# Optimization experiments

Measured on AMD Instinct MI355X. Metric: run time of the kernel, lower is better.

## Reference

```python
import jax, jax.numpy as jnp
import numpy as np

V, E, H2 = 32000, 512, 1024  # vocab, embed dim, lstm hidden (hidden_dim*2)
H = 512                      # attention inner dim (hidden_dim)
B, S = 64, 128
L = 2


def _lstm_cell(x, h, c, w_ih, w_hh, b_ih, b_hh):
    # PyTorch gate order: i, f, g, o
    gates = x @ w_ih.T + b_ih + h @ w_hh.T + b_hh
    i, f, g, o = jnp.split(gates, 4, axis=-1)
    i = jax.nn.sigmoid(i); f = jax.nn.sigmoid(f)
    g = jnp.tanh(g); o = jax.nn.sigmoid(o)
    c_new = f * c + i * g
    h_new = o * jnp.tanh(c_new)
    return h_new, c_new


def setup_inputs() -> dict:
    key = jax.random.key(0)
    ks = jax.random.split(key, 20)
    s = 0.05
    inp = {
        'input_token': jax.random.randint(ks[0], (B,), 0, V, dtype=jnp.int32),
        'hidden': jax.random.normal(ks[1], (L, B, H2), jnp.float32),
        'cell': jax.random.normal(ks[2], (L, B, H2), jnp.float32),
        'encoder_outputs': jax.random.normal(ks[3], (B, S, H2), jnp.float32),
        'mask': jax.random.randint(ks[4], (B, S), 0, 2, dtype=jnp.int32),
        'emb_table': jax.random.normal(ks[5], (V, E), jnp.float32) * s,
        'attn_w': jax.random.normal(ks[6], (H, 4 * H), jnp.float32) * s,
        'attn_b': jnp.zeros((H,), jnp.float32),
        'v_w': jax.random.normal(ks[7], (1, H), jnp.float32) * s,
        'w_ih0': jax.random.normal(ks[8], (4 * H2, E + H2), jnp.float32) * s,
        'w_hh0': jax.random.normal(ks[9], (4 * H2, H2), jnp.float32) * s,
        'b_ih0': jnp.zeros((4 * H2,), jnp.float32),
        'b_hh0': jnp.zeros((4 * H2,), jnp.float32),
        'w_ih1': jax.random.normal(ks[10], (4 * H2, H2), jnp.float32) * s,
        'w_hh1': jax.random.normal(ks[11], (4 * H2, H2), jnp.float32) * s,
        'b_ih1': jnp.zeros((4 * H2,), jnp.float32),
        'b_hh1': jnp.zeros((4 * H2,), jnp.float32),
        'fc_w': jax.random.normal(ks[12], (V, 4 * H + E), jnp.float32) * s,
        'fc_b': jnp.zeros((V,), jnp.float32),
    }
    return inp


def reference(input_token, hidden, cell, encoder_outputs, mask,
              emb_table, attn_w, attn_b, v_w,
              w_ih0, w_hh0, b_ih0, b_hh0,
              w_ih1, w_hh1, b_ih1, b_hh1,
              fc_w, fc_b):
    embedded = emb_table[input_token]                       # [B, E]
    h_top = hidden[-1]                                      # [B, 2H]
    # Bahdanau additive attention
    h_rep = jnp.broadcast_to(h_top[:, None, :], (B, S, H2))
    energy = jnp.tanh(jnp.concatenate([h_rep, encoder_outputs], axis=2) @ attn_w.T + attn_b)  # [B,S,H]
    attention = energy @ v_w[0]                             # [B, S]
    attention = jnp.where(mask == 0, jnp.float32(-1e10), attention)
    attn_weights = jax.nn.softmax(attention, axis=1)
    context = jnp.einsum('bs,bsd->bd', attn_weights, encoder_outputs)  # [B, 2H]
    # single-step 2-layer LSTM
    x = jnp.concatenate([embedded, context], axis=1)        # [B, E+2H]
    h0, c0 = _lstm_cell(x, hidden[0], cell[0], w_ih0, w_hh0, b_ih0, b_hh0)
    h1, c1 = _lstm_cell(h0, hidden[1], cell[1], w_ih1, w_hh1, b_ih1, b_hh1)
    new_hidden = jnp.stack([h0, h1])
    new_cell = jnp.stack([c0, c1])
    prediction = jnp.concatenate([h1, context, embedded], axis=1) @ fc_w.T + fc_b  # [B, V]
    return prediction, new_hidden, new_cell, attn_weights
```

## Files before the change

kernel.cpp:

```cpp
#include <hip/hip_runtime.h>


typedef __attribute__((ext_vector_type(8))) short bf16x8;
typedef __attribute__((ext_vector_type(4))) float f32x4;

__device__ __forceinline__ short f2bf(float f){
  __bf16 h = (__bf16)f;
  return __builtin_bit_cast(short, h);
}

__device__ __forceinline__ bf16x8 cvt8(float4 a, float4 b){
  bf16x8 r;
  r[0]=f2bf(a.x); r[1]=f2bf(a.y); r[2]=f2bf(a.z); r[3]=f2bf(a.w);
  r[4]=f2bf(b.x); r[5]=f2bf(b.y); r[6]=f2bf(b.z); r[7]=f2bf(b.w);
  return r;
}

__device__ __forceinline__ bf16x8 ld8_bf(const float* __restrict__ p){
  return cvt8(*(const float4*)p, *(const float4*)(p + 4));
}

__device__ __forceinline__ float fast_tanh(float x){
  x = fminf(fmaxf(x, -15.f), 15.f);
  float t = __expf(2.f * x);
  return (t - 1.f) / (t + 1.f);
}
__device__ __forceinline__ float fast_sig(float x){
  return 1.f / (1.f + __expf(-x));
}

__device__ __forceinline__ void stage16(const void* src, void* dst_lds){
  __builtin_amdgcn_global_load_lds(
      (const __attribute__((address_space(1))) void*)src,
      (__attribute__((address_space(3))) void*)dst_lds, 16, 0, 0);
}

__device__ __forceinline__ void gates_body(
    const short* __restrict__ A, int lda,
    const float* __restrict__ W1, int sW1, int K1,
    const float* __restrict__ W2, int sW2,
    float* __restrict__ Pplane, int N, int nb, int k0, char* smem)
{
  short* Al = (short*)smem;
  float* Wl = (float*)(smem + 32768);
  const int wv   = threadIdx.x >> 6;
  const int lane = threadIdx.x & 63;
  const int l15  = lane & 15;
  const int lg   = lane >> 4;

  const float* W; int sW, koff;
  if (k0 < K1){ W = W1; sW = sW1; koff = k0; }
  else        { W = W2; sW = sW2; koff = k0 - K1; }

  {
    const int r2  = lane >> 5;
    const int c16 = (lane & 31) * 16;
    #pragma unroll
    for (int i = 0; i < 8; ++i){
      int rbase = wv*16 + i*2;
      int row   = rbase + r2;
      const char* src = (const char*)A + (long)row*lda*2 + (long)k0*2
                        + (c16 ^ ((row & 7) << 4));
      stage16(src, (void*)(Al + rbase*256));
    }
  }

  auto STAGEW = [&](int bi, int kbase){
    #pragma unroll
    for (int i = 0; i < 4; ++i){
      int row = wv*16 + i*4 + lg;
      const char* src = (const char*)(W + (long)(nb + row)*sW + koff + kbase)
                        + ((l15*16) ^ ((row & 7) << 4));
      stage16(src, (void*)(Wl + bi*4096 + (wv*16 + i*4)*64));
    }
  };

  STAGEW(0, 0);
  STAGEW(1, 64);
  asm volatile("s_waitcnt vmcnt(8)" ::: "memory");
  asm volatile("s_barrier" ::: "memory");

  f32x4 acc[4];
  #pragma unroll
  for (int m = 0; m < 4; ++m) acc[m] = (f32x4){0.f,0.f,0.f,0.f};

  const int  rl = wv*16 + l15;
  const int  sw = (l15 & 7) << 4;
  const char* wbase = (const char*)Wl;
  const char* abase = (const char*)Al;

  auto COMPUTE = [&](int bi, int t){
    bf16x8 a[4][2];
    #pragma unroll
    for (int m = 0; m < 4; ++m)
      #pragma unroll
      for (int h = 0; h < 2; ++h){
        int cb = t*128 + h*64 + lg*16;
        a[m][h] = *(const bf16x8*)(abase + (m*16 + l15)*512 + (cb ^ sw));
      }
    const char* rb = wbase + bi*16384 + rl*256;
    float4 w00 = *(const float4*)(rb + ((lg*32      ) ^ sw));
    float4 w01 = *(const float4*)(rb + ((lg*32 + 16 ) ^ sw));
    float4 w10 = *(const float4*)(rb + ((lg*32 + 128) ^ sw));
    float4 w11 = *(const float4*)(rb + ((lg*32 + 144) ^ sw));
    bf16x8 wf0 = cvt8(w00, w01);
    bf16x8 wf1 = cvt8(w10, w11);
    #pragma unroll
    for (int m = 0; m < 4; ++m)
      acc[m] = __builtin_amdgcn_mfma_f32_16x16x32_bf16(a[m][0], wf0, acc[m], 0,0,0);
    #pragma unroll
    for (int m = 0; m < 4; ++m)
      acc[m] = __builtin_amdgcn_mfma_f32_16x16x32_bf16(a[m][1], wf1, acc[m], 0,0,0);
  };

  asm volatile("s_waitcnt vmcnt(4)" ::: "memory");
  COMPUTE(0, 0);
  STAGEW(2, 128);
  asm volatile("s_waitcnt vmcnt(4)" ::: "memory");
  COMPUTE(1, 1);
  STAGEW(0, 192);
  asm volatile("s_waitcnt vmcnt(4)" ::: "memory");
  COMPUTE(2, 2);
  asm volatile("s_waitcnt vmcnt(0)" ::: "memory");
  COMPUTE(0, 3);

  #pragma unroll
  for (int mt = 0; mt < 4; ++mt)
    #pragma unroll
    for (int r = 0; r < 4; ++r){
      int m = mt*16 + lg*4 + r;
      Pplane[(long)m * N + nb + wv*16 + l15] = acc[mt][r];
    }
}

__device__ __forceinline__ void fc_body(
    const short* __restrict__ A, int lda,
    const float* __restrict__ W, int sW, int NC,
    const float* __restrict__ addsrc, const float* __restrict__ bias,
    float* __restrict__ C, int N, int nb, char* smem)
{
  short* Al = (short*)smem;
  float* Wl = (float*)(smem + 32768);
  const int wv   = threadIdx.x >> 6;
  const int lane = threadIdx.x & 63;
  const int l15  = lane & 15;
  const int lg   = lane >> 4;

  auto STAGEA = [&](int c){
    short* dst = Al + (c & 1) * 8192;
    #pragma unroll
    for (int i = 0; i < 4; ++i){
      int rbase = wv*16 + i*4;
      int row   = rbase + lg;
      const char* src = (const char*)(A + (long)row*lda + c*128)
                        + ((l15*16) ^ ((row & 7) << 4));
      stage16(src, (void*)(dst + rbase*128));
    }
  };
  auto STAGEW = [&](int s){
    float* dst = Wl + (s % 3) * 4096;
    #pragma unroll
    for (int i = 0; i < 4; ++i){
      int row = wv*16 + i*4 + lg;
      const char* src = (const char*)(W + (long)(nb + row)*sW + s*64)
                        + ((l15*16) ^ ((row & 7) << 4));
      stage16(src, (void*)(dst + (wv*16 + i*4)*64));
    }
  };

  f32x4 acc[4];
  #pragma unroll
  for (int m = 0; m < 4; ++m) acc[m] = (f32x4){0.f,0.f,0.f,0.f};

  const int rl = wv*16 + l15;
  const int sw = (l15 & 7) << 4;

  auto COMPUTE = [&](int s){
    const char* abase = (const char*)(Al + ((s >> 1) & 1) * 8192);
    const int   kh    = (s & 1) * 128;
    bf16x8 a[4][2];
    #pragma unroll
    for (int m = 0; m < 4; ++m)
      #pragma unroll
      for (int h = 0; h < 2; ++h){
        int cb = kh + h*64 + lg*16;
        a[m][h] = *(const bf16x8*)(abase + (m*16 + l15)*256 + (cb ^ sw));
      }
    const char* rb = (const char*)(Wl + (s % 3)*4096) + rl*256;
    float4 w00 = *(const float4*)(rb + ((lg*32      ) ^ sw));
    float4 w01 = *(const float4*)(rb + ((lg*32 + 16 ) ^ sw));
    float4 w10 = *(const float4*)(rb + ((lg*32 + 128) ^ sw));
    float4 w11 = *(const float4*)(rb + ((lg*32 + 144) ^ sw));
    bf16x8 wf0 = cvt8(w00, w01);
    bf16x8 wf1 = cvt8(w10, w11);
    #pragma unroll
    for (int m = 0; m < 4; ++m)
      acc[m] = __builtin_amdgcn_mfma_f32_16x16x32_bf16(a[m][0], wf0, acc[m], 0,0,0);
    #pragma unroll
    for (int m = 0; m < 4; ++m)
      acc[m] = __builtin_amdgcn_mfma_f32_16x16x32_bf16(a[m][1], wf1, acc[m], 0,0,0);
  };

  STAGEA(0); STAGEW(0); STAGEW(1);
  asm volatile("s_waitcnt vmcnt(4)" ::: "memory");
  __builtin_amdgcn_s_barrier();

  STAGEA(1);
  COMPUTE(0);
  STAGEW(2);
  asm volatile("s_waitcnt vmcnt(4)" ::: "memory");
  COMPUTE(1);
  STAGEW(3);
  __builtin_amdgcn_s_barrier();

  for (int c = 1; c < NC-1; ++c){
    STAGEA(c+1);
    asm volatile("s_waitcnt vmcnt(8)" ::: "memory");
    COMPUTE(2*c);
    STAGEW(2*c+2);
    asm volatile("s_waitcnt vmcnt(4)" ::: "memory");
    COMPUTE(2*c+1);
    STAGEW(2*c+3);
    __builtin_amdgcn_s_barrier();
  }

  asm volatile("s_waitcnt vmcnt(4)" ::: "memory");
  COMPUTE(2*NC-2);
  asm volatile("s_waitcnt vmcnt(0)" ::: "memory");
  COMPUTE(2*NC-1);

  const int col = nb + wv*16 + l15;
  const float bn = bias ? bias[col] : 0.f;
  #pragma unroll
  for (int mt = 0; mt < 4; ++mt)
    #pragma unroll
    for (int r = 0; r < 4; ++r){
      int m = mt*16 + lg*4 + r;
      long idx = (long)m * N + col;
      float v = acc[mt][r] + bn;
      if (addsrc) v += addsrc[idx];
      C[idx] = v;
    }
}

__global__ __launch_bounds__(256) void prep_all(
    const int* __restrict__ tok, const float* __restrict__ emb,
    const float* __restrict__ hidden, const float* __restrict__ enc,
    const float* __restrict__ attn_w, const float* __restrict__ attn_b,
    short* __restrict__ encbf, short* __restrict__ Wbf,
    short* __restrict__ A0, short* __restrict__ A1, short* __restrict__ Zb,
    float* __restrict__ sco, float* __restrict__ hpr)
{
  const int bid = blockIdx.x, t = threadIdx.x;
  if (bid < 8){
    const int wv = t >> 6, lane = t & 63, l15 = lane & 15, lg = lane >> 4;
    const int nb = bid*64 + wv*16;
    const float* hrow = hidden + 65536;
    const float* wrow = attn_w + (long)(nb + l15)*2048 + lg*8;
    f32x4 acc[4] = {};
    bf16x8 wn  = ld8_bf(wrow);
    bf16x8 an0 = ld8_bf(hrow + l15*1024 + lg*8);
    bf16x8 an1 = ld8_bf(hrow + (16+l15)*1024 + lg*8);
    bf16x8 an2 = ld8_bf(hrow + (32+l15)*1024 + lg*8);
    bf16x8 an3 = ld8_bf(hrow + (48+l15)*1024 + lg*8);
    for (int kb = 32; kb < 1024; kb += 32){
      bf16x8 wc = wn, c0 = an0, c1 = an1, c2 = an2, c3 = an3;
      wn  = ld8_bf(wrow + kb);
      an0 = ld8_bf(hrow + l15*1024 + lg*8 + kb);
      an1 = ld8_bf(hrow + (16+l15)*1024 + lg*8 + kb);
      an2 = ld8_bf(hrow + (32+l15)*1024 + lg*8 + kb);
      an3 = ld8_bf(hrow + (48+l15)*1024 + lg*8 + kb);
      acc[0] = __builtin_amdgcn_mfma_f32_16x16x32_bf16(c0, wc, acc[0], 0,0,0);
      acc[1] = __builtin_amdgcn_mfma_f32_16x16x32_bf16(c1, wc, acc[1], 0,0,0);
      acc[2] = __builtin_amdgcn_mfma_f32_16x16x32_bf16(c2, wc, acc[2], 0,0,0);
      acc[3] = __builtin_amdgcn_mfma_f32_16x16x32_bf16(c3, wc, acc[3], 0,0,0);
    }
    acc[0] = __builtin_amdgcn_mfma_f32_16x16x32_bf16(an0, wn, acc[0], 0,0,0);
    acc[1] = __builtin_amdgcn_mfma_f32_16x16x32_bf16(an1, wn, acc[1], 0,0,0);
    acc[2] = __builtin_amdgcn_mfma_f32_16x16x32_bf16(an2, wn, acc[2], 0,0,0);
    acc[3] = __builtin_amdgcn_mfma_f32_16x16x32_bf16(an3, wn, acc[3], 0,0,0);
    const float bn = attn_b[nb + l15];
    #pragma unroll
    for (int mt = 0; mt < 4; ++mt)
      #pragma unroll
      for (int r = 0; r < 4; ++r)
        hpr[(mt*16 + lg*4 + r)*512 + nb + l15] = acc[mt][r] + bn;
  } else if (bid < 4104){
    long i = ((long)(bid-8)*256 + t)*8;
    *(bf16x8*)(encbf + i) = ld8_bf(enc + i);
  } else if (bid < 4360){
    int j = (bid-4104)*256 + t;
    int r = j >> 7, c = (j & 127)*8;
    *(bf16x8*)(Wbf + r*1024 + c) = ld8_bf(attn_w + (long)r*2048 + 1024 + c);
  } else if (bid < 4376){
    int j = (bid-4360)*256 + t;
    int b = j >> 6, e8 = (j & 63)*8;
    bf16x8 v = ld8_bf(emb + (long)tok[b]*512 + e8);
    *(bf16x8*)(A0 + b*2560 + e8) = v;
    *(bf16x8*)(Zb + b*2560 + 2048 + e8) = v;
  } else if (bid < 4408){
    int j = (bid-4376)*256 + t;
    int b = j >> 7, n8 = (j & 127)*8;
    *(bf16x8*)(A0 + b*2560 + 1536 + n8) = ld8_bf(hidden + (long)b*1024 + n8);
    *(bf16x8*)(A1 + b*2048 + 1024 + n8) = ld8_bf(hidden + 65536 + (long)b*1024 + n8);
  } else {
    int j = (bid-4408)*256 + t;
    float4 z = {0.f, 0.f, 0.f, 0.f};
    *(float4*)(sco + j*8) = z;
    *(float4*)(sco + j*8 + 4) = z;
  }
}

__global__ __launch_bounds__(256) void energy_lds(
    const short* __restrict__ encbf, const short* __restrict__ Wbf,
    const float* __restrict__ hpr, const float* __restrict__ v_w,
    float* __restrict__ scores)
{
  __shared__ short Ab[3][64*64];
  __shared__ short Bb[3][64*64];
  const int bx   = blockIdx.x;
  const int m3   = bx & 127, n3 = bx >> 7;
  const int wv   = threadIdx.x >> 6;
  const int lane = threadIdx.x & 63;
  const int l15  = lane & 15;
  const int lg   = lane >> 4;
  const int mb   = m3 * 64;
  const int nbg  = n3 * 64;
  const int nb   = nbg + wv * 16;
  const int b    = mb >> 7;

  const float hp = hpr[(long)b*512 + nb + l15];
  const float vn = v_w[nb + l15];

  const int srow = lane >> 3;
  const int scb  = (lane & 7) * 16;

  auto STAGE = [&](int c, int kb){
    short* da = Ab[c % 3];
    short* db = Bb[c % 3];
    #pragma unroll
    for (int i = 0; i < 2; ++i){
      int rbase = wv*16 + i*8;
      int row   = rbase + srow;
      int swz   = scb ^ ((row & 7) << 4);
      const char* sa = (const char*)(encbf + (long)(mb + row)*1024 + kb) + swz;
      stage16(sa, (void*)(da + rbase*64));
      const char* sb = (const char*)(Wbf + (long)(nbg + row)*1024 + kb) + swz;
      stage16(sb, (void*)(db + rbase*64));
    }
  };

  f32x4 acc[4] = {};
  const int brow = wv*16 + l15;
  const int bswz = (brow & 7) << 4;
  const int aswz = (l15 & 7) << 4;

  auto COMPUTE = [&](int c){
    const char* ab = (const char*)Ab[c % 3];
    const char* bb = (const char*)Bb[c % 3];
    #pragma unroll
    for (int h = 0; h < 2; ++h){
      const int colb = h*64 + lg*16;
      bf16x8 bf_ = *(const bf16x8*)(bb + brow*128 + (colb ^ bswz));
      #pragma unroll
      for (int m = 0; m < 4; ++m){
        const int arow = m*16 + l15;
        bf16x8 af = *(const bf16x8*)(ab + arow*128 + (colb ^ aswz));
        acc[m] = __builtin_amdgcn_mfma_f32_16x16x32_bf16(af, bf_, acc[m], 0,0,0);
      }
    }
  };

  STAGE(0, 0);
  STAGE(1, 64);
  for (int c = 0; c < 14; ++c){
    asm volatile("s_waitcnt vmcnt(4)" ::: "memory");
    __builtin_amdgcn_s_barrier();
    COMPUTE(c);
    STAGE(c+2, (c+2)*64);
  }
  asm volatile("s_waitcnt vmcnt(4)" ::: "memory");
  __builtin_amdgcn_s_barrier();
  COMPUTE(14);
  asm volatile("s_waitcnt vmcnt(0)" ::: "memory");
  __builtin_amdgcn_s_barrier();
  COMPUTE(15);

  #pragma unroll
  for (int mt = 0; mt < 4; ++mt){
    #pragma unroll
    for (int r = 0; r < 4; ++r){
      int m = mb + mt*16 + lg*4 + r;
      float e = fast_tanh(acc[mt][r] + hp) * vn;
      e += __shfl_xor(e, 1, 16);
      e += __shfl_xor(e, 2, 16);
      e += __shfl_xor(e, 4, 16);
      e += __shfl_xor(e, 8, 16);
      if (l15 == 0) atomicAdd(&scores[m], e);
    }
  }
}

__global__ __launch_bounds__(256) void ctxsm_k(
    const float* __restrict__ sco, const int* __restrict__ mask,
    const short* __restrict__ encbf, float* __restrict__ aw,
    short* __restrict__ A0, short* __restrict__ Zb)
{
  const int bb = blockIdx.x;
  const int t  = threadIdx.x;
  __shared__ float red[128];
  __shared__ float w[128];
  float v = 0.f;
  if (t < 128){
    v = sco[bb*128 + t];
    if (mask[bb*128 + t] == 0) v = -1e10f;
    red[t] = v;
  }
  __syncthreads();
  for (int d = 64; d > 0; d >>= 1){
    if (t < d) red[t] = fmaxf(red[t], red[t + d]);
    __syncthreads();
  }
  const float mx = red[0];
  __syncthreads();
  if (t < 128){
    float e = __expf(v - mx);
    w[t] = e; red[t] = e;
  }
  __syncthreads();
  for (int d = 64; d > 0; d >>= 1){
    if (t < d) red[t] += red[t + d];
    __syncthreads();
  }
  const float inv = 1.f / red[0];
  if (blockIdx.y == 0 && t < 128) aw[bb*128 + t] = w[t] * inv;

  const int dd = blockIdx.y * 256 + t;
  const unsigned short* e = (const unsigned short*)encbf + (long)bb*131072 + dd;
  float s0 = 0.f, s1 = 0.f, s2 = 0.f, s3 = 0.f;
  #pragma unroll 8
  for (int si = 0; si < 128; si += 4){
    s0 += w[si  ] * __builtin_bit_cast(float, (unsigned)e[(si  )*1024] << 16);
    s1 += w[si+1] * __builtin_bit_cast(float, (unsigned)e[(si+1)*1024] << 16);
    s2 += w[si+2] * __builtin_bit_cast(float, (unsigned)e[(si+2)*1024] << 16);
    s3 += w[si+3] * __builtin_bit_cast(float, (unsigned)e[(si+3)*1024] << 16);
  }
  float s = ((s0 + s1) + (s2 + s3)) * inv;
  short vbf = f2bf(s);
  A0[bb*2560 + 512  + dd] = vbf;
  Zb[bb*2560 + 1024 + dd] = vbf;
}

__global__ __launch_bounds__(256) void gemm_lds(
    const short* __restrict__ A, int lda,
    const float* __restrict__ W1, int sW1, int K1,
    const float* __restrict__ W2, int sW2,
    float* __restrict__ P, int N)
{
  __shared__ char smem[81920];
  gates_body(A, lda, W1, sW1, K1, W2, sW2,
             P + (long)blockIdx.y * 64 * N, N,
             blockIdx.x * 64, blockIdx.y * 256, smem);
}

__global__ __launch_bounds__(256) void combo_k(
    const short* __restrict__ A0, const float* __restrict__ w_ih0,
    const float* __restrict__ w_hh0, float* __restrict__ Pb,
    const short* __restrict__ Zb, const float* __restrict__ fc_w,
    float* __restrict__ predP)
{
  __shared__ char smem[81920];
  if (blockIdx.x < 500){
    fc_body(Zb + 1024, 2560, fc_w + 1024, 2560, 12, nullptr, nullptr,
            predP, 32000, blockIdx.x * 64, smem);
  } else {
    int b2 = blockIdx.x - 500;
    gates_body(A0, 2560, w_ih0, 1536, 1536, w_hh0, 1024,
               Pb + (long)(b2 >> 6) * 262144, 4096,
               (b2 & 63) * 64, (b2 >> 6) * 256, smem);
  }
}

__global__ __launch_bounds__(256) void fc_final(
    const short* __restrict__ Zb, const float* __restrict__ fc_w,
    const float* __restrict__ predP, const float* __restrict__ fc_b,
    float* __restrict__ pred)
{
  __shared__ char smem[81920];
  fc_body(Zb, 2560, fc_w, 2560, 8, predP, fc_b, pred, 32000,
          blockIdx.x * 64, smem);
}

template<int KS>
__global__ __launch_bounds__(256) void lstm_k(
    const float* __restrict__ P,
    const float* __restrict__ bi, const float* __restrict__ bh,
    const float* __restrict__ c_prev,
    float* __restrict__ h_out, float* __restrict__ c_out,
    short* __restrict__ h_bf, int bf_stride)
{
  const int i = blockIdx.x * 256 + threadIdx.x;
  const int b = i >> 10, n = i & 1023;
  float g4[4];
  #pragma unroll
  for (int gi = 0; gi < 4; ++gi){
    int col = gi*1024 + n;
    float s = bi[col] + bh[col];
    const float* p = P + (long)b*4096 + col;
    #pragma unroll
    for (int sl = 0; sl < KS; ++sl) s += p[(long)sl * 262144];
    g4[gi] = s;
  }
  float iv = fast_sig (g4[0]);
  float fv = fast_sig (g4[1]);
  float gv = fast_tanh(g4[2]);
  float ov = fast_sig (g4[3]);
  float c = fv * c_prev[i] + iv * gv;
  float h = ov * fast_tanh(c);
  c_out[i] = c;
  h_out[i] = h;
  h_bf[(long)b * bf_stride + n] = f2bf(h);
}

extern "C" void kernel_launch(void* const* d_in, const int* in_sizes, int n_in,
                              void* d_out, int out_size, void* d_ws, size_t ws_size,
                              hipStream_t stream)
{
  const int*   tok    = (const int*)  d_in[0];
  const float* hidden = (const float*)d_in[1];
  const float* cell   = (const float*)d_in[2];
  const float* enc    = (const float*)d_in[3];
  const int*   mask   = (const int*)  d_in[4];
  const float* emb    = (const float*)d_in[5];
  const float* attn_w = (const float*)d_in[6];
  const float* attn_b = (const float*)d_in[7];
  const float* v_w    = (const float*)d_in[8];
  const float* w_ih0  = (const float*)d_in[9];
  const float* w_hh0  = (const float*)d_in[10];
  const float* b_ih0  = (const float*)d_in[11];
  const float* b_hh0  = (const float*)d_in[12];
  const float* w_ih1  = (const float*)d_in[13];
  const float* w_hh1  = (const float*)d_in[14];
  const float* b_ih1  = (const float*)d_in[15];
  const float* b_hh1  = (const float*)d_in[16];
  const float* fc_w   = (const float*)d_in[17];
  const float* fc_b   = (const float*)d_in[18];

  float* out  = (float*)d_out;
  float* pred = out;
  float* nh   = out + 2048000;
  float* nc   = out + 2179072;
  float* aw   = out + 2310144;

  char*  wsb   = (char*)d_ws;
  short* encbf = (short*)(wsb + 0);
  short* Wbf   = (short*)(wsb + 16777216);
  short* A0    = (short*)(wsb + 17825792);
  short* A1    = (short*)(wsb + 18153472);
  short* Zb    = (short*)(wsb + 18415616);
  float* sco   = (float*)(wsb + 18743296);
  float* hpr   = (float*)(wsb + 18776064);
  float* Pb    = (float*)(wsb + 18907136);
  float* predP = (float*)(wsb + 29392896);

  prep_all<<<4412, 256, 0, stream>>>(tok, emb, hidden, enc, attn_w, attn_b,
                                     encbf, Wbf, A0, A1, Zb, sco, hpr);

  energy_lds<<<1024, 256, 0, stream>>>(encbf, Wbf, hpr, v_w, sco);

  ctxsm_k<<<dim3(64, 4), 256, 0, stream>>>(sco, mask, encbf, aw, A0, Zb);

  combo_k<<<1140, 256, 0, stream>>>(A0, w_ih0, w_hh0, Pb, Zb, fc_w, predP);

  lstm_k<10><<<256, 256, 0, stream>>>(Pb, b_ih0, b_hh0, cell,
                                      nh, nc, A1, 2048);

  gemm_lds<<<dim3(64, 8), 256, 0, stream>>>(A1, 2048,
                                            w_ih1, 1024, 1024, w_hh1, 1024,
                                            Pb, 4096);
  lstm_k<8><<<256, 256, 0, stream>>>(Pb, b_ih1, b_hh1, cell + 65536,
                                     nh + 65536, nc + 65536, Zb, 2560);

  fc_final<<<500, 256, 0, stream>>>(Zb, fc_w, predP, fc_b, pred);
}
```

Before: 175.3 us.

## Overlap layer-1 hidden-state GEMM with layer-0 gates, unsplit final FC

New measurement: 169.7 us. 1.03x faster.

```diff
diff --git a/kernel.cpp b/kernel.cpp
--- a/kernel.cpp
+++ b/kernel.cpp
@@ -136,7 +136,7 @@
 __device__ __forceinline__ void fc_body(
     const short* __restrict__ A, int lda,
     const float* __restrict__ W, int sW, int NC,
-    const float* __restrict__ addsrc, const float* __restrict__ bias,
+    const float* __restrict__ bias,
     float* __restrict__ C, int N, int nb, char* smem)
 {
   short* Al = (short*)smem;
@@ -230,16 +230,13 @@
   COMPUTE(2*NC-1);
 
   const int col = nb + wv*16 + l15;
-  const float bn = bias ? bias[col] : 0.f;
+  const float bn = bias[col];
   #pragma unroll
   for (int mt = 0; mt < 4; ++mt)
     #pragma unroll
     for (int r = 0; r < 4; ++r){
       int m = mt*16 + lg*4 + r;
-      long idx = (long)m * N + col;
-      float v = acc[mt][r] + bn;
-      if (addsrc) v += addsrc[idx];
-      C[idx] = v;
+      C[(long)m * N + col] = acc[mt][r] + bn;
     }
 }
 
@@ -451,44 +448,41 @@
   Zb[bb*2560 + 1024 + dd] = vbf;
 }
 
-__global__ __launch_bounds__(256) void gemm_lds(
-    const short* __restrict__ A, int lda,
-    const float* __restrict__ W1, int sW1, int K1,
-    const float* __restrict__ W2, int sW2,
-    float* __restrict__ P, int N)
-{
-  __shared__ char smem[81920];
-  gates_body(A, lda, W1, sW1, K1, W2, sW2,
-             P + (long)blockIdx.y * 64 * N, N,
-             blockIdx.x * 64, blockIdx.y * 256, smem);
-}
-
-__global__ __launch_bounds__(256) void combo_k(
+__global__ __launch_bounds__(256) void gates01_k(
     const short* __restrict__ A0, const float* __restrict__ w_ih0,
     const float* __restrict__ w_hh0, float* __restrict__ Pb,
+    const short* __restrict__ A1, const float* __restrict__ w_ih1,
+    const float* __restrict__ w_hh1, float* __restrict__ Pb1)
+{
+  __shared__ char smem[81920];
+  if (blockIdx.x < 640){
+    int sl = blockIdx.x >> 6, ct = blockIdx.x & 63;
+    gates_body(A0, 2560, w_ih0, 1536, 1536, w_hh0, 1024,
+               Pb + (long)sl * 262144, 4096, ct * 64, sl * 256, smem);
+  } else {
+    int b2 = blockIdx.x - 640;
+    int sl = 4 + (b2 >> 6), ct = b2 & 63;
+    gates_body(A1, 2048, w_ih1, 1024, 1024, w_hh1, 1024,
+               Pb1 + (long)sl * 262144, 4096, ct * 64, sl * 256, smem);
+  }
+}
+
+__global__ __launch_bounds__(256) void gates1a_k(
+    const short* __restrict__ A1, const float* __restrict__ w_ih1,
+    float* __restrict__ Pb1)
+{
+  __shared__ char smem[81920];
+  gates_body(A1, 2048, w_ih1, 1024, 1<<30, nullptr, 0,
+             Pb1 + (long)blockIdx.y * 262144, 4096,
+             blockIdx.x * 64, blockIdx.y * 256, smem);
+}
+
+__global__ __launch_bounds__(256) void fc_k(
     const short* __restrict__ Zb, const float* __restrict__ fc_w,
-    float* __restrict__ predP)
+    const float* __restrict__ fc_b, float* __restrict__ pred)
 {
   __shared__ char smem[81920];
-  if (blockIdx.x < 500){
-    fc_body(Zb + 1024, 2560, fc_w + 1024, 2560, 12, nullptr, nullptr,
-            predP, 32000, blockIdx.x * 64, smem);
-  } else {
-    int b2 = blockIdx.x - 500;
-    gates_body(A0, 2560, w_ih0, 1536, 1536, w_hh0, 1024,
-               Pb + (long)(b2 >> 6) * 262144, 4096,
-               (b2 & 63) * 64, (b2 >> 6) * 256, smem);
-  }
-}
-
-__global__ __launch_bounds__(256) void fc_final(
-    const short* __restrict__ Zb, const float* __restrict__ fc_w,
-    const float* __restrict__ predP, const float* __restrict__ fc_b,
-    float* __restrict__ pred)
-{
-  __shared__ char smem[81920];
-  fc_body(Zb, 2560, fc_w, 2560, 8, predP, fc_b, pred, 32000,
-          blockIdx.x * 64, smem);
+  fc_body(Zb, 2560, fc_w, 2560, 20, fc_b, pred, 32000, blockIdx.x * 64, smem);
 }
 
 template<int KS>
@@ -561,7 +555,7 @@
   float* sco   = (float*)(wsb + 18743296);
   float* hpr   = (float*)(wsb + 18776064);
   float* Pb    = (float*)(wsb + 18907136);
-  float* predP = (float*)(wsb + 29392896);
+  float* Pb1   = (float*)(wsb + 29392896);
 
   prep_all<<<4412, 256, 0, stream>>>(tok, emb, hidden, enc, attn_w, attn_b,
                                      encbf, Wbf, A0, A1, Zb, sco, hpr);
@@ -570,16 +564,16 @@
 
   ctxsm_k<<<dim3(64, 4), 256, 0, stream>>>(sco, mask, encbf, aw, A0, Zb);
 
-  combo_k<<<1140, 256, 0, stream>>>(A0, w_ih0, w_hh0, Pb, Zb, fc_w, predP);
+  gates01_k<<<896, 256, 0, stream>>>(A0, w_ih0, w_hh0, Pb,
+                                     A1, w_ih1, w_hh1, Pb1);
 
   lstm_k<10><<<256, 256, 0, stream>>>(Pb, b_ih0, b_hh0, cell,
                                       nh, nc, A1, 2048);
 
-  gemm_lds<<<dim3(64, 8), 256, 0, stream>>>(A1, 2048,
-                                            w_ih1, 1024, 1024, w_hh1, 1024,
-                                            Pb, 4096);
-  lstm_k<8><<<256, 256, 0, stream>>>(Pb, b_ih1, b_hh1, cell + 65536,
+  gates1a_k<<<dim3(64, 4), 256, 0, stream>>>(A1, w_ih1, Pb1);
+
+  lstm_k<8><<<256, 256, 0, stream>>>(Pb1, b_ih1, b_hh1, cell + 65536,
                                      nh + 65536, nc + 65536, Zb, 2560);
 
-  fc_final<<<500, 256, 0, stream>>>(Zb, fc_w, predP, fc_b, pred);
-}
+  fc_k<<<500, 256, 0, stream>>>(Zb, fc_w, fc_b, pred);
+}
```
